# Performance work log

Measured on AMD Instinct MI355X. Metric: run time of the kernel, lower is better.

## Reference

```python
import jax, jax.numpy as jnp
import numpy as np
import math

D_MODEL = 512
SLOPE = 0.5  # slope_init, not trainable


def setup_inputs() -> dict:
    key = jax.random.key(0)
    k1, k2, k3, k4 = jax.random.split(key, 4)
    B, S, D = 4, 4096, D_MODEL
    x = jax.random.normal(k1, (B, S, D), dtype=jnp.float32)
    # nn.Linear(d, d): weight is [d, d]; query_key weight used as x @ W (no transpose, bias unused)
    lim = 1.0 / math.sqrt(D)
    W_qk = jax.random.uniform(k2, (D, D), jnp.float32, -lim, lim)
    W_v = jax.random.uniform(k3, (D, D), jnp.float32, -lim, lim)
    b_v = jax.random.uniform(k4, (D,), jnp.float32, -lim, lim)
    return {"x": x, "W_qk": W_qk, "W_v": W_v, "b_v": b_v}


def reference(x, W_qk, W_v, b_v):
    B, S, D = x.shape
    scale = 1.0 / math.sqrt(D)
    # scores[b,i,j] = (x @ W_qk @ x^T) * scale   (torch: x @ weight @ x.transpose)
    scores = jnp.einsum('bid,de,bje->bij', x, W_qk, x) * scale
    # ALiBi bias: (j - i) * slope
    i = jnp.arange(S, dtype=x.dtype)[:, None]
    j = jnp.arange(S, dtype=x.dtype)[None, :]
    scores = scores + (j - i) * jnp.asarray(SLOPE, x.dtype)
    # causal mask: strict upper triangle -> -inf
    causal = j > i  # [S, S] bool
    scores = jnp.where(causal, -jnp.inf, scores)
    attn = jax.nn.softmax(scores, axis=-1)
    # value_linear: x @ W_v^T + b_v (standard nn.Linear)
    v = jnp.einsum('bjd,ed->bje', x, W_v) + b_v
    return jnp.einsum('bij,bje->bie', attn, v)
```

## Files before the change

kernel.cpp:

```cpp
#include <hip/hip_runtime.h>
#include <math.h>

#define D_MODEL 512
#define SEQ     4096
#define BATCH   4
#define BS      (BATCH * SEQ)

typedef __attribute__((ext_vector_type(8))) short  short8;
typedef __attribute__((ext_vector_type(4))) float  float4v;

#define GAS __attribute__((address_space(1)))
#define LAS __attribute__((address_space(3)))

__device__ __forceinline__ void gld_lds16(const void* g, void* l) {
  __builtin_amdgcn_global_load_lds((const GAS unsigned int*)g,
                                   (LAS unsigned int*)l, 16, 0, 0);
}

__device__ __forceinline__ unsigned short bf16r(float f) {
  unsigned int u = __builtin_bit_cast(unsigned int, f);
  u += 0x7fffu + ((u >> 16) & 1u);
  return (unsigned short)(u >> 16);
}

__device__ __forceinline__ uint4 pack8(float4 a, float4 b) {
  uint4 o;
  o.x = bf16r(a.x) | ((unsigned)bf16r(a.y) << 16);
  o.y = bf16r(a.z) | ((unsigned)bf16r(a.w) << 16);
  o.z = bf16r(b.x) | ((unsigned)bf16r(b.y) << 16);
  o.w = bf16r(b.z) | ((unsigned)bf16r(b.w) << 16);
  return o;
}

__global__ __launch_bounds__(256) void cvt_w(const float* __restrict__ Wqk,
                                             unsigned short* __restrict__ Wqkt,
                                             const float* __restrict__ Wv,
                                             unsigned short* __restrict__ Wvb,
                                             const float* __restrict__ x,
                                             unsigned short* __restrict__ xb) {
  if (blockIdx.x < 64) {
    __shared__ float tile[64][65];
    const int bx = blockIdx.x & 7;
    const int by = blockIdx.x >> 3;
    const int tx = threadIdx.x & 63;
    const int ty = threadIdx.x >> 6;
    for (int r = ty; r < 64; r += 4)
      tile[r][tx] = Wqk[(size_t)(by * 64 + r) * D_MODEL + bx * 64 + tx];
    __syncthreads();
    for (int r = ty; r < 64; r += 4)
      Wqkt[(size_t)(bx * 64 + r) * D_MODEL + by * 64 + tx] = bf16r(tile[tx][r]);
  } else if (blockIdx.x < 192) {
    const int idx = ((blockIdx.x - 64) * 256 + threadIdx.x) * 8;
    const float4 a = *(const float4*)(Wv + idx);
    const float4 b = *(const float4*)(Wv + idx + 4);
    *(uint4*)(Wvb + idx) = pack8(a, b);
  } else {
    const size_t idx = ((size_t)(blockIdx.x - 192) * 256 + threadIdx.x) * 8;
    const float4 a = *(const float4*)(x + idx);
    const float4 b = *(const float4*)(x + idx + 4);
    *(uint4*)(xb + idx) = pack8(a, b);
  }
}

template <bool VT>
__device__ __forceinline__ void gemm_path(const unsigned short* __restrict__ xb,
                                          const unsigned short* __restrict__ Wgt,
                                          const float* __restrict__ bias,
                                          unsigned short* __restrict__ C,
                                          int a0, float alpha,
                                          unsigned short* Ws, unsigned short* As) {
  const int t    = threadIdx.x;
  const int w    = t >> 6;
  const int lane = t & 63;
  const int q    = lane >> 4;
  const int c    = lane & 15;
  const int wbase = w * 128;
  const int sw   = c & 7;

  constexpr int NI = VT ? 8 : 4;
  constexpr int NJ = VT ? 4 : 8;

  float4v acc[NI][NJ];
#pragma unroll
  for (int i = 0; i < NI; ++i)
#pragma unroll
    for (int j = 0; j < NJ; ++j) acc[i][j] = (float4v){0.f, 0.f, 0.f, 0.f};

  for (int k0 = 0; k0 < D_MODEL; k0 += 64) {
#pragma unroll
    for (int it = 0; it < 16; ++it) {
      const int idx = it * 256 + t;
      const int r   = idx >> 3;
      const int s   = idx & 7;
      gld_lds16(Wgt + (size_t)r * D_MODEL + k0 + ((s ^ (r & 7)) * 8),
                &Ws[idx * 8]);
    }
#pragma unroll
    for (int it = 0; it < 2; ++it) {
      const int idx = it * 256 + t;
      const int r   = idx >> 3;
      const int s   = idx & 7;
      gld_lds16(xb + (size_t)(a0 + r) * D_MODEL + k0 + ((s ^ (r & 7)) * 8),
                &As[idx * 8]);
    }
    __syncthreads();

#pragma unroll
    for (int kc = 0; kc < 2; ++kc) {
      const int slot = ((kc * 4 + q) ^ sw) * 8;
      short8 af[NI], bf[NJ];
#pragma unroll
      for (int i = 0; i < NI; ++i) {
        const int row = VT ? (wbase + i * 16 + c) : (i * 16 + c);
        const unsigned short* src = (VT ? Ws : As) + row * 64 + slot;
        af[i] = *(const short8*)src;
      }
#pragma unroll
      for (int j = 0; j < NJ; ++j) {
        const int row = VT ? (j * 16 + c) : (wbase + j * 16 + c);
        const unsigned short* src = (VT ? As : Ws) + row * 64 + slot;
        bf[j] = *(const short8*)src;
      }
#pragma unroll
      for (int i = 0; i < NI; ++i)
#pragma unroll
        for (int j = 0; j < NJ; ++j)
          acc[i][j] = __builtin_amdgcn_mfma_f32_16x16x32_bf16(af[i], bf[j], acc[i][j], 0, 0, 0);
    }
    __syncthreads();
  }

  if (!VT) {
#pragma unroll
    for (int i = 0; i < NI; ++i)
#pragma unroll
      for (int tt = 0; tt < 4; ++tt) {
        const int row = a0 + i * 16 + 4 * q + tt;
#pragma unroll
        for (int j = 0; j < NJ; ++j)
          C[(size_t)row * D_MODEL + wbase + j * 16 + c] = bf16r(alpha * acc[i][j][tt]);
      }
  } else {
#pragma unroll
    for (int i = 0; i < NI; ++i)
#pragma unroll
      for (int tt = 0; tt < 4; ++tt) {
        const int dim = wbase + i * 16 + 4 * q + tt;
        const float bv = bias[dim];
#pragma unroll
        for (int j = 0; j < NJ; ++j)
          C[(size_t)dim * BS + a0 + j * 16 + c] = bf16r(acc[i][j][tt] + bv);
      }
  }
}

__global__ __launch_bounds__(256, 2) void qv_gemm(const unsigned short* __restrict__ xb,
                                                  const unsigned short* __restrict__ Wqkt,
                                                  const unsigned short* __restrict__ Wvb,
                                                  const float* __restrict__ bv,
                                                  unsigned short* __restrict__ Qb,
                                                  unsigned short* __restrict__ Vt,
                                                  float scale) {
  __shared__ unsigned short Ws[512 * 64];
  __shared__ unsigned short As[64 * 64];
  if (blockIdx.x < 256)
    gemm_path<false>(xb, Wqkt, nullptr, Qb, blockIdx.x * 64, scale, Ws, As);
  else
    gemm_path<true>(xb, Wvb, bv, Vt, (blockIdx.x - 256) * 64, 1.0f, Ws, As);
}

__global__ __launch_bounds__(128) void attn_tile(const unsigned short* __restrict__ Q,
                                                 const unsigned short* __restrict__ Kx,
                                                 const unsigned short* __restrict__ Vt,
                                                 float* __restrict__ out) {
  constexpr int PLD = 72;
  __shared__ unsigned short pls[16 * PLD];
  __shared__ float lm[2][16], ls[2][16];

  const int t    = threadIdx.x;
  const int h    = t >> 6;
  const int lane = t & 63;
  const int q    = lane >> 4;
  const int c    = lane & 15;

  const int tile = ((blockIdx.x & 7) << 7) + (blockIdx.x >> 3);
  const int r0   = tile << 4;
  const int b    = r0 >> 12;
  const int i0   = r0 & (SEQ - 1);
  const int jb   = i0 - 48;

  short8 qf[16];
  {
    const unsigned short* qp = Q + (size_t)(r0 + c) * D_MODEL + q * 8;
#pragma unroll
    for (int ch = 0; ch < 16; ++ch) qf[ch] = *(const short8*)(qp + ch * 32);
  }

  float4v sacc[2];
  sacc[0] = (float4v){0.f, 0.f, 0.f, 0.f};
  sacc[1] = (float4v){0.f, 0.f, 0.f, 0.f};
#pragma unroll
  for (int s = 0; s < 2; ++s) {
    const int sj = 2 * h + s;
    if (jb + 16 * sj + 15 < 0) continue;
    int krow = jb + 16 * sj + c;
    if (krow < 0) krow = 0;
    const unsigned short* kr = Kx + ((size_t)(b << 12) + krow) * D_MODEL + q * 8;
    float4v sv = sacc[s];
#pragma unroll
    for (int ch = 0; ch < 16; ++ch)
      sv = __builtin_amdgcn_mfma_f32_16x16x32_bf16(qf[ch], *(const short8*)(kr + ch * 32), sv, 0, 0, 0);
    sacc[s] = sv;
  }

  const unsigned short* vbase = Vt + (size_t)(h * 256 + c) * BS + (b << 12);
  const bool ch0 = (jb + 31 >= 0);
  short8 vf0[16];
  if (ch0) {
    int kk = jb + q * 8;
    if (kk < 0) kk = 0;
    const unsigned short* vb = vbase + kk;
#pragma unroll
    for (int dt = 0; dt < 16; ++dt) vf0[dt] = *(const short8*)(vb + (size_t)dt * 16 * BS);
  }

  float tmax[4] = {-1e30f, -1e30f, -1e30f, -1e30f};
#pragma unroll
  for (int s = 0; s < 2; ++s)
#pragma unroll
    for (int tt = 0; tt < 4; ++tt) {
      const int jl = jb + 16 * (2 * h + s) + c;
      const int il = i0 + 4 * q + tt;
      float sv = sacc[s][tt];
      sv = (jl < 0 || jl > il) ? -1e30f : sv + 0.5f * (float)(jl - il);
      sacc[s][tt] = sv;
      tmax[tt] = fmaxf(tmax[tt], sv);
    }
#pragma unroll
  for (int tt = 0; tt < 4; ++tt) {
    float v = tmax[tt];
    v = fmaxf(v, __shfl_xor(v, 1, 64));
    v = fmaxf(v, __shfl_xor(v, 2, 64));
    v = fmaxf(v, __shfl_xor(v, 4, 64));
    v = fmaxf(v, __shfl_xor(v, 8, 64));
    tmax[tt] = v;
  }
  if (c == 0) {
#pragma unroll
    for (int tt = 0; tt < 4; ++tt) lm[h][4 * q + tt] = tmax[tt];
  }
  __syncthreads();

  float m[4];
#pragma unroll
  for (int tt = 0; tt < 4; ++tt)
    m[tt] = fmaxf(lm[0][4 * q + tt], lm[1][4 * q + tt]);

  float rsum[4] = {0.f, 0.f, 0.f, 0.f};
#pragma unroll
  for (int s = 0; s < 2; ++s)
#pragma unroll
    for (int tt = 0; tt < 4; ++tt) {
      const float p = __expf(sacc[s][tt] - m[tt]);
      rsum[tt] += p;
      pls[(4 * q + tt) * PLD + (2 * h + s) * 16 + c] = bf16r(p);
    }
#pragma unroll
  for (int tt = 0; tt < 4; ++tt) {
    float v = rsum[tt];
    v += __shfl_xor(v, 1, 64);
    v += __shfl_xor(v, 2, 64);
    v += __shfl_xor(v, 4, 64);
    v += __shfl_xor(v, 8, 64);
    rsum[tt] = v;
  }
  if (c == 0) {
#pragma unroll
    for (int tt = 0; tt < 4; ++tt) ls[h][4 * q + tt] = rsum[tt];
  }
  __syncthreads();

  float l[4];
#pragma unroll
  for (int tt = 0; tt < 4; ++tt)
    l[tt] = ls[0][4 * q + tt] + ls[1][4 * q + tt];

  float4v oacc[16];
#pragma unroll
  for (int dt = 0; dt < 16; ++dt) oacc[dt] = (float4v){0.f, 0.f, 0.f, 0.f};

  if (ch0) {
    const short8 pa = *(const short8*)&pls[c * PLD + q * 8];
#pragma unroll
    for (int dt = 0; dt < 16; ++dt)
      oacc[dt] = __builtin_amdgcn_mfma_f32_16x16x32_bf16(pa, vf0[dt], oacc[dt], 0, 0, 0);
  }
  {
    const short8 pa = *(const short8*)&pls[c * PLD + 32 + q * 8];
    int kk = jb + 32 + q * 8;
    if (kk < 0) kk = 0;
    const unsigned short* vb = vbase + kk;
#pragma unroll
    for (int dt = 0; dt < 16; ++dt) {
      const short8 vf = *(const short8*)(vb + (size_t)dt * 16 * BS);
      oacc[dt] = __builtin_amdgcn_mfma_f32_16x16x32_bf16(pa, vf, oacc[dt], 0, 0, 0);
    }
  }

  float inv[4];
#pragma unroll
  for (int tt = 0; tt < 4; ++tt) inv[tt] = 1.0f / l[tt];
#pragma unroll
  for (int dt = 0; dt < 16; ++dt)
#pragma unroll
    for (int tt = 0; tt < 4; ++tt)
      out[(size_t)(r0 + 4 * q + tt) * D_MODEL + h * 256 + dt * 16 + c] =
          oacc[dt][tt] * inv[tt];
}

extern "C" void kernel_launch(void* const* d_in, const int* in_sizes, int n_in,
                              void* d_out, int out_size, void* d_ws,
                              size_t ws_size, hipStream_t stream) {
  const float* x   = (const float*)d_in[0];
  const float* Wqk = (const float*)d_in[1];
  const float* Wv  = (const float*)d_in[2];
  const float* bv  = (const float*)d_in[3];
  float* out = (float*)d_out;

  unsigned short* xb   = (unsigned short*)d_ws;
  unsigned short* Qb   = xb + (size_t)BS * D_MODEL;
  unsigned short* Vt   = Qb + (size_t)BS * D_MODEL;
  unsigned short* Wqkt = Vt + (size_t)BS * D_MODEL;
  unsigned short* Wvb  = Wqkt + (size_t)D_MODEL * D_MODEL;

  const float scale = 1.0f / sqrtf((float)D_MODEL);

  cvt_w<<<dim3(192 + (BS * D_MODEL / 2048)), dim3(256), 0, stream>>>(Wqk, Wqkt, Wv, Wvb, x, xb);
  qv_gemm<<<dim3(512), dim3(256), 0, stream>>>(xb, Wqkt, Wvb, bv, Qb, Vt, scale);
  attn_tile<<<dim3(BS / 16), dim3(128), 0, stream>>>(Qb, xb, Vt, out);
}
```

Before: 132.8 us.

## Retile QV GEMM into 256x256 blocks with double-buffered LDS staging

Replaces the 64-row by 512-column GEMM tiles with 256x256 output tiles computed by 512-thread blocks, giving each weight and activation load more reuse. K slabs are now double-buffered in LDS, so the next slab is prefetched while the current one is multiplied. Q and V tiles are dispatched by block index within a single kernel. The grid drops to 256 blocks with one block per CU and a 128KB LDS footprint, which lowers occupancy and may leave some CUs idle.

```diff
diff --git a/kernel.cpp b/kernel.cpp
--- a/kernel.cpp
+++ b/kernel.cpp
@@ -62,111 +62,103 @@
   }
 }
 
-template <bool VT>
-__device__ __forceinline__ void gemm_path(const unsigned short* __restrict__ xb,
-                                          const unsigned short* __restrict__ Wgt,
-                                          const float* __restrict__ bias,
-                                          unsigned short* __restrict__ C,
-                                          int a0, float alpha,
-                                          unsigned short* Ws, unsigned short* As) {
-  const int t    = threadIdx.x;
-  const int w    = t >> 6;
-  const int lane = t & 63;
-  const int q    = lane >> 4;
-  const int c    = lane & 15;
-  const int wbase = w * 128;
-  const int sw   = c & 7;
-
-  constexpr int NI = VT ? 8 : 4;
-  constexpr int NJ = VT ? 4 : 8;
-
-  float4v acc[NI][NJ];
-#pragma unroll
-  for (int i = 0; i < NI; ++i)
-#pragma unroll
-    for (int j = 0; j < NJ; ++j) acc[i][j] = (float4v){0.f, 0.f, 0.f, 0.f};
-
-  for (int k0 = 0; k0 < D_MODEL; k0 += 64) {
-#pragma unroll
-    for (int it = 0; it < 16; ++it) {
-      const int idx = it * 256 + t;
-      const int r   = idx >> 3;
-      const int s   = idx & 7;
-      gld_lds16(Wgt + (size_t)r * D_MODEL + k0 + ((s ^ (r & 7)) * 8),
-                &Ws[idx * 8]);
-    }
-#pragma unroll
-    for (int it = 0; it < 2; ++it) {
-      const int idx = it * 256 + t;
-      const int r   = idx >> 3;
-      const int s   = idx & 7;
-      gld_lds16(xb + (size_t)(a0 + r) * D_MODEL + k0 + ((s ^ (r & 7)) * 8),
-                &As[idx * 8]);
-    }
-    __syncthreads();
-
-#pragma unroll
-    for (int kc = 0; kc < 2; ++kc) {
-      const int slot = ((kc * 4 + q) ^ sw) * 8;
-      short8 af[NI], bf[NJ];
-#pragma unroll
-      for (int i = 0; i < NI; ++i) {
-        const int row = VT ? (wbase + i * 16 + c) : (i * 16 + c);
-        const unsigned short* src = (VT ? Ws : As) + row * 64 + slot;
-        af[i] = *(const short8*)src;
-      }
-#pragma unroll
-      for (int j = 0; j < NJ; ++j) {
-        const int row = VT ? (j * 16 + c) : (wbase + j * 16 + c);
-        const unsigned short* src = (VT ? As : Ws) + row * 64 + slot;
-        bf[j] = *(const short8*)src;
-      }
-#pragma unroll
-      for (int i = 0; i < NI; ++i)
-#pragma unroll
-        for (int j = 0; j < NJ; ++j)
-          acc[i][j] = __builtin_amdgcn_mfma_f32_16x16x32_bf16(af[i], bf[j], acc[i][j], 0, 0, 0);
-    }
-    __syncthreads();
-  }
-
-  if (!VT) {
-#pragma unroll
-    for (int i = 0; i < NI; ++i)
-#pragma unroll
-      for (int tt = 0; tt < 4; ++tt) {
-        const int row = a0 + i * 16 + 4 * q + tt;
-#pragma unroll
-        for (int j = 0; j < NJ; ++j)
-          C[(size_t)row * D_MODEL + wbase + j * 16 + c] = bf16r(alpha * acc[i][j][tt]);
-      }
-  } else {
-#pragma unroll
-    for (int i = 0; i < NI; ++i)
-#pragma unroll
-      for (int tt = 0; tt < 4; ++tt) {
-        const int dim = wbase + i * 16 + 4 * q + tt;
-        const float bv = bias[dim];
-#pragma unroll
-        for (int j = 0; j < NJ; ++j)
-          C[(size_t)dim * BS + a0 + j * 16 + c] = bf16r(acc[i][j][tt] + bv);
-      }
-  }
-}
-
-__global__ __launch_bounds__(256, 2) void qv_gemm(const unsigned short* __restrict__ xb,
+__global__ __launch_bounds__(512, 1) void qv_gemm(const unsigned short* __restrict__ xb,
                                                   const unsigned short* __restrict__ Wqkt,
                                                   const unsigned short* __restrict__ Wvb,
                                                   const float* __restrict__ bv,
                                                   unsigned short* __restrict__ Qb,
                                                   unsigned short* __restrict__ Vt,
                                                   float scale) {
-  __shared__ unsigned short Ws[512 * 64];
-  __shared__ unsigned short As[64 * 64];
-  if (blockIdx.x < 256)
-    gemm_path<false>(xb, Wqkt, nullptr, Qb, blockIdx.x * 64, scale, Ws, As);
-  else
-    gemm_path<true>(xb, Wvb, bv, Vt, (blockIdx.x - 256) * 64, 1.0f, Ws, As);
+  __shared__ unsigned short As[2][256 * 64];
+  __shared__ unsigned short Bs[2][256 * 64];
+
+  const int t    = threadIdx.x;
+  const int w    = t >> 6;
+  const int lane = t & 63;
+  const int q    = lane >> 4;
+  const int c    = lane & 15;
+  const int wr   = w >> 1;
+  const int wc   = w & 1;
+  const int sw   = c & 7;
+
+  const int mt = blockIdx.x & 63;
+  const int nt = blockIdx.x >> 6;
+  const int a0 = mt * 256;
+  const int b0 = (nt & 1) * 256;
+  const bool vt = (nt >= 2);
+  const unsigned short* __restrict__ Wgt = vt ? Wvb : Wqkt;
+
+  float4v acc[4][8];
+#pragma unroll
+  for (int i = 0; i < 4; ++i)
+#pragma unroll
+    for (int j = 0; j < 8; ++j) acc[i][j] = (float4v){0.f, 0.f, 0.f, 0.f};
+
+  auto stage = [&](int buf, int k0) {
+#pragma unroll
+    for (int it = 0; it < 4; ++it) {
+      const int idx = it * 512 + t;
+      const int r   = idx >> 3;
+      const int ss  = idx & 7;
+      const int ko  = k0 + ((ss ^ (r & 7)) << 3);
+      gld_lds16(xb + (size_t)(a0 + r) * D_MODEL + ko, &As[buf][idx * 8]);
+      gld_lds16(Wgt + (size_t)(b0 + r) * D_MODEL + ko, &Bs[buf][idx * 8]);
+    }
+  };
+
+  stage(0, 0);
+  __syncthreads();
+
+  for (int slab = 0; slab < 8; ++slab) {
+    const int buf = slab & 1;
+    if (slab < 7) stage(buf ^ 1, (slab + 1) * 64);
+
+    const unsigned short* SA = vt ? Bs[buf] : As[buf];
+    const unsigned short* SB = vt ? As[buf] : Bs[buf];
+
+#pragma unroll
+    for (int kc = 0; kc < 2; ++kc) {
+      const int slot = ((kc * 4 + q) ^ sw) * 8;
+      short8 af[4], bf[8];
+#pragma unroll
+      for (int i = 0; i < 4; ++i)
+        af[i] = *(const short8*)&SA[(wr * 64 + i * 16 + c) * 64 + slot];
+#pragma unroll
+      for (int j = 0; j < 8; ++j)
+        bf[j] = *(const short8*)&SB[(wc * 128 + j * 16 + c) * 64 + slot];
+#pragma unroll
+      for (int i = 0; i < 4; ++i)
+#pragma unroll
+        for (int j = 0; j < 8; ++j)
+          acc[i][j] = __builtin_amdgcn_mfma_f32_16x16x32_bf16(af[i], bf[j], acc[i][j], 0, 0, 0);
+    }
+    __syncthreads();
+  }
+
+  if (!vt) {
+#pragma unroll
+    for (int i = 0; i < 4; ++i)
+#pragma unroll
+      for (int tt = 0; tt < 4; ++tt) {
+        const int row = a0 + wr * 64 + i * 16 + 4 * q + tt;
+        const int cb  = nt * 256 + wc * 128;
+#pragma unroll
+        for (int j = 0; j < 8; ++j)
+          Qb[(size_t)row * D_MODEL + cb + j * 16 + c] = bf16r(scale * acc[i][j][tt]);
+      }
+  } else {
+#pragma unroll
+    for (int i = 0; i < 4; ++i)
+#pragma unroll
+      for (int tt = 0; tt < 4; ++tt) {
+        const int dim = (nt - 2) * 256 + wr * 64 + i * 16 + 4 * q + tt;
+        const float bvv = bv[dim];
+        const int kb  = a0 + wc * 128;
+#pragma unroll
+        for (int j = 0; j < 8; ++j)
+          Vt[(size_t)dim * BS + kb + j * 16 + c] = bf16r(acc[i][j][tt] + bvv);
+      }
+  }
 }
 
 __global__ __launch_bounds__(128) void attn_tile(const unsigned short* __restrict__ Q,
@@ -336,6 +328,6 @@
   const float scale = 1.0f / sqrtf((float)D_MODEL);
 
   cvt_w<<<dim3(192 + (BS * D_MODEL / 2048)), dim3(256), 0, stream>>>(Wqk, Wqkt, Wv, Wvb, x, xb);
-  qv_gemm<<<dim3(512), dim3(256), 0, stream>>>(xb, Wqkt, Wvb, bv, Qb, Vt, scale);
+  qv_gemm<<<dim3(256), dim3(512), 0, stream>>>(xb, Wqkt, Wvb, bv, Qb, Vt, scale);
   attn_tile<<<dim3(BS / 16), dim3(128), 0, stream>>>(Qb, xb, Vt, out);
 }
```

After: 132.8 us. Within noise of the previous version (-0.0%).
